# Optimization experiments

Measured on AMD Instinct MI355X. Metric: run time of the kernel, lower is better.

## Reference

```python
import jax, jax.numpy as jnp
import numpy as np

N = 100_000      # amino-acid nodes
E = 1_600_000    # edges per relation (avg degree 16)
D = 128          # input_dim
H = 128          # hidden_dim
L = 2            # num_layers
EPS = 1e-5       # BatchNorm eps


def setup_inputs() -> dict:
    key = jax.random.key(0)
    ks = jax.random.split(key, 20)
    inp = {
        "x": jax.random.normal(ks[0], (N, D), dtype=jnp.float32),
        "src_residue": jax.random.randint(ks[1], (E,), 0, N, dtype=jnp.int32),
        "dst_residue": jax.random.randint(ks[2], (E,), 0, N, dtype=jnp.int32),
        "src_seq": jax.random.randint(ks[3], (E,), 0, N, dtype=jnp.int32),
        "dst_seq": jax.random.randint(ks[4], (E,), 0, N, dtype=jnp.int32),
        "src_knn": jax.random.randint(ks[5], (E,), 0, N, dtype=jnp.int32),
        "dst_knn": jax.random.randint(ks[6], (E,), 0, N, dtype=jnp.int32),
        # GraphConv weights: 3 relations per layer; layer0 in=D, layer1 in=H
        "Wg0": jax.random.normal(ks[7], (3, D, H), dtype=jnp.float32) * (1.0 / np.sqrt(D)),
        "bg0": jnp.zeros((3, H), dtype=jnp.float32),
        "Wg1": jax.random.normal(ks[8], (3, H, H), dtype=jnp.float32) * (1.0 / np.sqrt(H)),
        "bg1": jnp.zeros((3, H), dtype=jnp.float32),
        # FC per layer
        "Wfc": jax.random.normal(ks[9], (L, H, H), dtype=jnp.float32) * (1.0 / np.sqrt(H)),
        "bfc": jax.random.normal(ks[10], (L, H), dtype=jnp.float32) * 0.01,
        # BatchNorm1d (eval mode: running stats)
        "bn_gamma": 1.0 + 0.1 * jax.random.normal(ks[11], (L, H), dtype=jnp.float32),
        "bn_beta": 0.1 * jax.random.normal(ks[12], (L, H), dtype=jnp.float32),
        "bn_mean": 0.1 * jax.random.normal(ks[13], (L, H), dtype=jnp.float32),
        "bn_var": jax.random.uniform(ks[14], (L, H), dtype=jnp.float32, minval=0.5, maxval=1.5),
    }
    return inp


def reference(x, src_residue, dst_residue, src_seq, dst_seq, src_knn, dst_knn,
              Wg0, bg0, Wg1, bg1, Wfc, bfc, bn_gamma, bn_beta, bn_mean, bn_var):
    n = x.shape[0]
    edges = [(src_residue, dst_residue), (src_seq, dst_seq), (src_knn, dst_knn)]

    def gconv(h, src, dst, W, b):
        # DGL GraphConv, norm='both': D_dst^{-1/2} A D_src^{-1/2} h W + b
        ones = jnp.ones(src.shape, h.dtype)
        deg_out = jnp.maximum(jax.ops.segment_sum(ones, src, num_segments=n), 1.0)
        deg_in = jnp.maximum(jax.ops.segment_sum(ones, dst, num_segments=n), 1.0)
        hn = h * jax.lax.rsqrt(deg_out)[:, None]
        agg = jax.ops.segment_sum(hn[src], dst, num_segments=n)  # [N, d] gather+scatter
        agg = agg * jax.lax.rsqrt(deg_in)[:, None]
        return agg @ W + b

    h = x
    layer_weights = [(Wg0, bg0), (Wg1, bg1)]
    for i, (Wg, bg) in enumerate(layer_weights):
        # HeteroGraphConv with aggregate='sum' over 3 relations
        out = gconv(h, edges[0][0], edges[0][1], Wg[0], bg[0])
        out = out + gconv(h, edges[1][0], edges[1][1], Wg[1], bg[1])
        out = out + gconv(h, edges[2][0], edges[2][1], Wg[2], bg[2])
        y = jax.nn.relu(out @ Wfc[i] + bfc[i])
        # BatchNorm1d (eval: running stats); dropout is identity in eval mode
        h = (y - bn_mean[i]) * jax.lax.rsqrt(bn_var[i] + EPS) * bn_gamma[i] + bn_beta[i]
    return h
```

## Files before the change

kernel.cpp:

```cpp
#include <hip/hip_runtime.h>
#include <stdint.h>

#define NN 100000
#define NE 1600000
#define NE4 (NE / 4)
#define NNP1 100008
#define NBK 196
#define NSL 64

typedef __attribute__((ext_vector_type(8))) short bfrag;
typedef __attribute__((ext_vector_type(4))) float ffrag;

__device__ __forceinline__ uint16_t f2bf(float f) {
  uint32_t u = __float_as_uint(f);
  u += 0x7fff + ((u >> 16) & 1);
  return (uint16_t)(u >> 16);
}
__device__ __forceinline__ uint32_t pack2(float a, float b) {
  return (uint32_t)f2bf(a) | ((uint32_t)f2bf(b) << 16);
}

__global__ void k_cast_x(const float* __restrict__ x, uint32_t* __restrict__ h) {
  int n = NN * 64;
  for (int i = blockIdx.x * blockDim.x + threadIdx.x; i < n; i += gridDim.x * blockDim.x) {
    float2 v = ((const float2*)x)[i];
    h[i] = pack2(v.x, v.y);
  }
}

__global__ void k_prep_w(const float* __restrict__ Wg0, const float* __restrict__ Wg1,
                         const float* __restrict__ Wfc, uint16_t* __restrict__ wswz) {
  int idx = blockIdx.x * 256 + threadIdx.x;
  int m = idx >> 14;
  int rem = idx & 16383;
  int j = rem & 7;
  int lane = (rem >> 3) & 63;
  int f = rem >> 9;
  int t = f >> 3, ct = f & 7;
  int k = t * 32 + (lane >> 4) * 8 + j;
  int n = ct * 16 + (lane & 15);
  const float* src = (m < 3) ? (Wg0 + m * 16384)
                   : (m < 6) ? (Wg1 + (m - 3) * 16384)
                             : (Wfc + (m - 6) * 16384);
  wswz[idx] = f2bf(src[k * 128 + n]);
}

__global__ void k_prep_consts(const float* __restrict__ bg0, const float* __restrict__ bg1,
                              const float* __restrict__ Wfc, const float* __restrict__ bfc,
                              const float* __restrict__ gamma, const float* __restrict__ beta,
                              const float* __restrict__ mean, const float* __restrict__ var,
                              float* __restrict__ cst) {
  int tid = threadIdx.x;
  int l = tid >> 7, n = tid & 127;
  const float* bg = l ? bg1 : bg0;
  float acc = bfc[l * 128 + n];
  for (int k = 0; k < 128; k++) {
    float bsum = bg[k] + bg[128 + k] + bg[256 + k];
    acc += bsum * Wfc[l * 16384 + k * 128 + n];
  }
  cst[tid] = acc;
  float g = gamma[tid] * rsqrtf(var[tid] + 1e-5f);
  cst[256 + tid] = g;
  cst[512 + tid] = beta[tid] - mean[tid] * g;
}

__global__ void k_bhist(const int* __restrict__ s0, const int* __restrict__ s1,
                        const int* __restrict__ s2, const int* __restrict__ d0,
                        const int* __restrict__ d1, const int* __restrict__ d2,
                        uint32_t* __restrict__ bh) {
  int r = blockIdx.y, blk = blockIdx.x, t = threadIdx.x;
  __shared__ uint32_t hD[NBK], hS[NBK];
  for (int i = t; i < NBK; i += 256) { hD[i] = 0; hS[i] = 0; }
  __syncthreads();
  const int4* sp = (const int4*)((r == 0) ? s0 : (r == 1) ? s1 : s2);
  const int4* dp = (const int4*)((r == 0) ? d0 : (r == 1) ? d1 : d2);
  int base = blk * (NE4 / NSL);
  for (int i = t; i < NE4 / NSL; i += 256) {
    int4 s = sp[base + i];
    int4 d = dp[base + i];
    atomicAdd(&hD[d.x >> 9], 1u); atomicAdd(&hD[d.y >> 9], 1u);
    atomicAdd(&hD[d.z >> 9], 1u); atomicAdd(&hD[d.w >> 9], 1u);
    atomicAdd(&hS[s.x >> 9], 1u); atomicAdd(&hS[s.y >> 9], 1u);
    atomicAdd(&hS[s.z >> 9], 1u); atomicAdd(&hS[s.w >> 9], 1u);
  }
  __syncthreads();
  for (int i = t; i < NBK; i += 256) {
    if (hD[i]) atomicAdd(&bh[r * NBK + i], hD[i]);
    if (hS[i]) atomicAdd(&bh[(3 + r) * NBK + i], hS[i]);
  }
}

__global__ void k_bscan(const uint32_t* __restrict__ bh, int* __restrict__ bases,
                        uint32_t* __restrict__ cur, int* __restrict__ rowptr) {
  int seg = blockIdx.x, t = threadIdx.x;
  int lane = t & 63, wid = t >> 6;
  int v = (t < NBK) ? (int)bh[seg * NBK + t] : 0;
  int x = v;
#pragma unroll
  for (int o = 1; o < 64; o <<= 1) { int y = __shfl_up(x, o); if (lane >= o) x += y; }
  __shared__ int ws[4];
  if (lane == 63) ws[wid] = x;
  __syncthreads();
  int woff = 0;
  for (int i = 0; i < wid; i++) woff += ws[i];
  int incl = woff + x, excl = incl - v;
  if (t < NBK) { bases[seg * (NBK + 1) + t] = excl; cur[seg * NBK + t] = (uint32_t)excl; }
  if (t == 255) bases[seg * (NBK + 1) + NBK] = incl;
  if (seg < 3 && t == 0) rowptr[seg * NNP1 + NN] = NE;
}

__global__ void k_bscatter(const int* __restrict__ s0, const int* __restrict__ s1,
                           const int* __restrict__ s2, const int* __restrict__ d0,
                           const int* __restrict__ d1, const int* __restrict__ d2,
                           uint32_t* __restrict__ cur, uint32_t* __restrict__ pairs,
                           uint16_t* __restrict__ srcs) {
  int r = blockIdx.y, blk = blockIdx.x, t = threadIdx.x;
  __shared__ uint32_t hD[NBK], hS[NBK];
  for (int i = t; i < NBK; i += 256) { hD[i] = 0; hS[i] = 0; }
  __syncthreads();
  const int4* sp = (const int4*)((r == 0) ? s0 : (r == 1) ? s1 : s2);
  const int4* dp = (const int4*)((r == 0) ? d0 : (r == 1) ? d1 : d2);
  int base = blk * (NE4 / NSL);
  for (int i = t; i < NE4 / NSL; i += 256) {
    int4 s = sp[base + i];
    int4 d = dp[base + i];
    atomicAdd(&hD[d.x >> 9], 1u); atomicAdd(&hD[d.y >> 9], 1u);
    atomicAdd(&hD[d.z >> 9], 1u); atomicAdd(&hD[d.w >> 9], 1u);
    atomicAdd(&hS[s.x >> 9], 1u); atomicAdd(&hS[s.y >> 9], 1u);
    atomicAdd(&hS[s.z >> 9], 1u); atomicAdd(&hS[s.w >> 9], 1u);
  }
  __syncthreads();
  for (int i = t; i < NBK; i += 256) {
    hD[i] = atomicAdd(&cur[r * NBK + i], hD[i]);
    hS[i] = atomicAdd(&cur[(3 + r) * NBK + i], hS[i]);
  }
  __syncthreads();
  uint32_t* pr = pairs + (size_t)r * NE;
  uint16_t* sr = srcs + (size_t)r * NE;
#define SCAT1(S, D) { \
    uint32_t p = atomicAdd(&hD[(D) >> 9], 1u); \
    pr[p] = (uint32_t)(((D) & 511) << 17) | (uint32_t)(S); \
    uint32_t q = atomicAdd(&hS[(S) >> 9], 1u); \
    sr[q] = (uint16_t)((S) & 511); }
  for (int i = t; i < NE4 / NSL; i += 256) {
    int4 s = sp[base + i];
    int4 d = dp[base + i];
    SCAT1(s.x, d.x) SCAT1(s.y, d.y) SCAT1(s.z, d.z) SCAT1(s.w, d.w)
  }
#undef SCAT1
}

__global__ void k_bucket_csr(const uint32_t* __restrict__ pairs, const int* __restrict__ bases,
                             int* __restrict__ rowptr, float* __restrict__ s_in,
                             int* __restrict__ col) {
  int b = blockIdx.x, r = blockIdx.y, t = threadIdx.x;
  int node0 = b << 9;
  int nc = min(512, NN - node0);
  int rb = bases[r * (NBK + 1) + b];
  int m = bases[r * (NBK + 1) + b + 1] - rb;
  __shared__ int cnt[512];
  __shared__ int exc[512];
  __shared__ int ws[4];
  cnt[t] = 0; cnt[t + 256] = 0;
  __syncthreads();
  const uint32_t* pp = pairs + (size_t)r * NE + rb;
  for (int i = t; i < m; i += 256) atomicAdd(&cnt[pp[i] >> 17], 1);
  __syncthreads();
  int v0 = cnt[2 * t], v1 = cnt[2 * t + 1];
  int s = v0 + v1, x = s;
  int lane = t & 63, wid = t >> 6;
#pragma unroll
  for (int o = 1; o < 64; o <<= 1) { int y = __shfl_up(x, o); if (lane >= o) x += y; }
  if (lane == 63) ws[wid] = x;
  __syncthreads();
  int woff = 0;
  for (int i = 0; i < wid; i++) woff += ws[i];
  int e0 = woff + x - s;
  exc[2 * t] = e0;
  exc[2 * t + 1] = e0 + v0;
  __syncthreads();
  for (int i = t; i < nc; i += 256) {
    rowptr[r * NNP1 + node0 + i] = rb + exc[i];
    s_in[r * NN + node0 + i] = rsqrtf((float)(cnt[i] < 1 ? 1 : cnt[i]));
  }
  __syncthreads();
  int* cl = col + (size_t)r * NE + rb;
  for (int i = t; i < m; i += 256) {
    uint32_t e = pp[i];
    int p = atomicAdd(&exc[e >> 17], 1);
    cl[p] = (int)(e & 0x1FFFF);
  }
}

__global__ void k_bucket_sout(const uint16_t* __restrict__ srcs, const int* __restrict__ bases,
                              float* __restrict__ s_out) {
  int b = blockIdx.x, r = blockIdx.y, t = threadIdx.x;
  int node0 = b << 9;
  int nc = min(512, NN - node0);
  int rb = bases[(3 + r) * (NBK + 1) + b];
  int m = bases[(3 + r) * (NBK + 1) + b + 1] - rb;
  __shared__ int cnt[512];
  cnt[t] = 0; cnt[t + 256] = 0;
  __syncthreads();
  const uint16_t* pp = srcs + (size_t)r * NE + rb;
  for (int i = t; i < m; i += 256) atomicAdd(&cnt[pp[i]], 1);
  __syncthreads();
  for (int i = t; i < nc; i += 256)
    s_out[r * NN + node0 + i] = rsqrtf((float)(cnt[i] < 1 ? 1 : cnt[i]));
}

__global__ void k_aggregate(const uint32_t* __restrict__ h, const int* __restrict__ rowptr,
                            const int* __restrict__ col, const float* __restrict__ s_out,
                            const float* __restrict__ s_in, uint32_t* __restrict__ agg) {
  int r = blockIdx.y;
  int node = blockIdx.x * 4 + (threadIdx.x >> 6);
  int lane = threadIdx.x & 63;
  const int* rp = rowptr + r * NNP1;
  int beg = rp[node], end = rp[node + 1];
  const int* cl = col + (size_t)r * NE;
  const float* so = s_out + r * NN;
  float a0 = 0.f, a1 = 0.f;
  for (int base = beg; base < end; base += 64) {
    int idx = base + lane;
    int sv = 0; int wb = 0;
    if (idx < end) { sv = cl[idx]; wb = __float_as_int(so[sv]); }
    int cnt = min(64, end - base);
    int cnt8 = (cnt + 7) & ~7;
    for (int j = 0; j < cnt8; j += 8) {
      uint32_t hv[8]; float ww[8];
#pragma unroll
      for (int u = 0; u < 8; u++) {
        int ss = __builtin_amdgcn_readlane(sv, j + u);
        ww[u] = __int_as_float(__builtin_amdgcn_readlane(wb, j + u));
        hv[u] = h[(size_t)ss * 64 + lane];
      }
#pragma unroll
      for (int u = 0; u < 8; u++) {
        a0 = fmaf(__uint_as_float(hv[u] << 16), ww[u], a0);
        a1 = fmaf(__uint_as_float(hv[u] & 0xffff0000u), ww[u], a1);
      }
    }
  }
  float sc = s_in[r * NN + node];
  agg[((size_t)r * NN + node) * 64 + lane] = pack2(a0 * sc, a1 * sc);
}

__global__ __launch_bounds__(256, 2) void k_gconv_mm(const uint32_t* __restrict__ agg,
                                                     const short* __restrict__ wswz,
                                                     int wbase, uint16_t* __restrict__ P) {
  int r = blockIdx.y;
  int lane = threadIdx.x & 63;
  int wid = threadIdx.x >> 6;
  int q = lane >> 4, n0 = lane & 15;
  const bfrag* wp = (const bfrag*)(wswz + (size_t)(wbase + r) * 16384);
  bfrag B[32];
#pragma unroll
  for (int f = 0; f < 32; f++) B[f] = wp[f * 64 + lane];
  const uint32_t* A = agg + (size_t)r * NN * 64;
  uint16_t* Pr = P + (size_t)r * NN * 128;
  const int ntiles = NN / 16;
  for (int tile = blockIdx.x * 4 + wid; tile < ntiles; tile += gridDim.x * 4) {
    int arow = tile * 16 + n0;
    bfrag a[4];
#pragma unroll
    for (int t = 0; t < 4; t++)
      a[t] = *(const bfrag*)(A + (size_t)arow * 64 + t * 16 + q * 4);
    ffrag acc[8];
#pragma unroll
    for (int ct = 0; ct < 8; ct++) {
      ffrag c = {0.f, 0.f, 0.f, 0.f};
#pragma unroll
      for (int t = 0; t < 4; t++)
        c = __builtin_amdgcn_mfma_f32_16x16x32_bf16(a[t], B[t * 8 + ct], c, 0, 0, 0);
      acc[ct] = c;
    }
    int orow = tile * 16 + q * 4;
#pragma unroll
    for (int ct = 0; ct < 8; ct++)
#pragma unroll
      for (int i = 0; i < 4; i++)
        Pr[(size_t)(orow + i) * 128 + ct * 16 + n0] = f2bf(acc[ct][i]);
  }
}

__global__ __launch_bounds__(256, 2) void k_fc(const uint32_t* __restrict__ P,
                                               const short* __restrict__ wswz, int m,
                                               const float* __restrict__ cst, int l,
                                               uint16_t* __restrict__ hout,
                                               float* __restrict__ fout, int wf32) {
  int lane = threadIdx.x & 63;
  int wid = threadIdx.x >> 6;
  int q = lane >> 4, n0 = lane & 15;
  const bfrag* wp = (const bfrag*)(wswz + (size_t)m * 16384);
  bfrag B[32];
#pragma unroll
  for (int f = 0; f < 32; f++) B[f] = wp[f * 64 + lane];
  float bb[8], gg[8], b2v[8];
#pragma unroll
  for (int ct = 0; ct < 8; ct++) {
    int c = l * 128 + ct * 16 + n0;
    bb[ct] = cst[c];
    gg[ct] = cst[256 + c];
    b2v[ct] = cst[512 + c];
  }
  const int ntiles = NN / 16;
  for (int tile = blockIdx.x * 4 + wid; tile < ntiles; tile += gridDim.x * 4) {
    int arow = tile * 16 + n0;
    ffrag acc[8];
#pragma unroll
    for (int ct = 0; ct < 8; ct++) acc[ct] = (ffrag){0.f, 0.f, 0.f, 0.f};
    for (int rr = 0; rr < 3; rr++) {
      const uint32_t* A = P + (size_t)rr * NN * 64;
      bfrag a[4];
#pragma unroll
      for (int t = 0; t < 4; t++)
        a[t] = *(const bfrag*)(A + (size_t)arow * 64 + t * 16 + q * 4);
#pragma unroll
      for (int ct = 0; ct < 8; ct++) {
#pragma unroll
        for (int t = 0; t < 4; t++)
          acc[ct] = __builtin_amdgcn_mfma_f32_16x16x32_bf16(a[t], B[t * 8 + ct], acc[ct], 0, 0, 0);
      }
    }
    int orow = tile * 16 + q * 4;
#pragma unroll
    for (int ct = 0; ct < 8; ct++) {
#pragma unroll
      for (int i = 0; i < 4; i++) {
        float y = acc[ct][i] + bb[ct];
        y = fmaxf(y, 0.f);
        float hv = fmaf(y, gg[ct], b2v[ct]);
        size_t oi = (size_t)(orow + i) * 128 + ct * 16 + n0;
        if (wf32) fout[oi] = hv;
        else hout[oi] = f2bf(hv);
      }
    }
  }
}

extern "C" void kernel_launch(void* const* d_in, const int* in_sizes, int n_in,
                              void* d_out, int out_size, void* d_ws, size_t ws_size,
                              hipStream_t stream) {
  const float* x = (const float*)d_in[0];
  const int* s0 = (const int*)d_in[1]; const int* d0 = (const int*)d_in[2];
  const int* s1 = (const int*)d_in[3]; const int* d1 = (const int*)d_in[4];
  const int* s2 = (const int*)d_in[5]; const int* d2 = (const int*)d_in[6];
  const float* Wg0 = (const float*)d_in[7];
  const float* bg0 = (const float*)d_in[8];
  const float* Wg1 = (const float*)d_in[9];
  const float* bg1 = (const float*)d_in[10];
  const float* Wfc = (const float*)d_in[11];
  const float* bfc = (const float*)d_in[12];
  const float* gamma = (const float*)d_in[13];
  const float* beta = (const float*)d_in[14];
  const float* mean = (const float*)d_in[15];
  const float* var = (const float*)d_in[16];

  char* ws = (char*)d_ws;
  size_t off = 0;
  auto alloc = [&](size_t bytes) { size_t o = off; off = (off + bytes + 255) & ~(size_t)255; return o; };
  size_t o_bh    = alloc((size_t)6 * NBK * 4);
  size_t o_bases = alloc((size_t)6 * (NBK + 1) * 4);
  size_t o_cur   = alloc((size_t)6 * NBK * 4);
  size_t o_sin   = alloc((size_t)3 * NN * 4);
  size_t o_sout  = alloc((size_t)3 * NN * 4);
  size_t o_rp    = alloc((size_t)3 * NNP1 * 4);
  size_t o_col   = alloc((size_t)3 * NE * 4);
  size_t o_wswz  = alloc((size_t)131072 * 2);
  size_t o_cst   = alloc((size_t)768 * 4);
  size_t o_h     = alloc((size_t)NN * 128 * 2);
  size_t o_agg   = alloc((size_t)3 * NN * 128 * 2);
  size_t o_P     = alloc((size_t)3 * NN * 128 * 2);
  (void)ws_size; (void)in_sizes; (void)n_in; (void)out_size;

  uint32_t* bh   = (uint32_t*)(ws + o_bh);
  int* bases     = (int*)(ws + o_bases);
  uint32_t* cur  = (uint32_t*)(ws + o_cur);
  float* s_in    = (float*)(ws + o_sin);
  float* s_out   = (float*)(ws + o_sout);
  int* rowptr    = (int*)(ws + o_rp);
  int* col       = (int*)(ws + o_col);
  uint16_t* wswz = (uint16_t*)(ws + o_wswz);
  float* cst     = (float*)(ws + o_cst);
  uint32_t* h    = (uint32_t*)(ws + o_h);
  uint32_t* agg  = (uint32_t*)(ws + o_agg);
  uint16_t* P    = (uint16_t*)(ws + o_P);
  uint32_t* pairs = (uint32_t*)(ws + o_agg);
  uint16_t* srcs  = (uint16_t*)(ws + o_agg + (size_t)3 * NE * 4);

  hipMemsetAsync(ws + o_bh, 0, (size_t)6 * NBK * 4, stream);

  k_cast_x<<<2048, 256, 0, stream>>>(x, h);
  k_prep_w<<<512, 256, 0, stream>>>(Wg0, Wg1, Wfc, wswz);
  k_prep_consts<<<1, 256, 0, stream>>>(bg0, bg1, Wfc, bfc, gamma, beta, mean, var, cst);
  k_bhist<<<dim3(NSL, 3), 256, 0, stream>>>(s0, s1, s2, d0, d1, d2, bh);
  k_bscan<<<6, 256, 0, stream>>>(bh, bases, cur, rowptr);
  k_bscatter<<<dim3(NSL, 3), 256, 0, stream>>>(s0, s1, s2, d0, d1, d2, cur, pairs, srcs);
  k_bucket_csr<<<dim3(NBK, 3), 256, 0, stream>>>(pairs, bases, rowptr, s_in, col);
  k_bucket_sout<<<dim3(NBK, 3), 256, 0, stream>>>(srcs, bases, s_out);

  for (int l = 0; l < 2; l++) {
    k_aggregate<<<dim3(25000, 3), 256, 0, stream>>>(h, rowptr, col, s_out, s_in, agg);
    k_gconv_mm<<<dim3(256, 3), 256, 0, stream>>>(agg, (const short*)wswz, 3 * l, P);
    k_fc<<<256, 256, 0, stream>>>((const uint32_t*)P, (const short*)wswz, 6 + l, cst, l,
                                  (uint16_t*)h, (float*)d_out, l);
  }
}
```

Before: 747.7 us.

## Fold GraphConv weights into FC weights and pack edge norms into CSR

```diff
diff --git a/kernel.cpp b/kernel.cpp
--- a/kernel.cpp
+++ b/kernel.cpp
@@ -28,21 +28,34 @@
   }
 }
 
-__global__ void k_prep_w(const float* __restrict__ Wg0, const float* __restrict__ Wg1,
-                         const float* __restrict__ Wfc, uint16_t* __restrict__ wswz) {
+__global__ void k_matmul_wc(const float* __restrict__ Wg0, const float* __restrict__ Wg1,
+                            const float* __restrict__ Wfc, float* __restrict__ Wc) {
+  int b = blockIdx.x;
+  int m = b >> 2, kq = b & 3;
+  int l = m / 3, rel = m % 3;
+  int t = threadIdx.x;
+  int n = t & 127, kh = t >> 7;
+  int k0 = kq * 32 + kh * 16;
+  const float* Wg = (l ? Wg1 : Wg0) + rel * 16384;
+  const float* Wf = Wfc + (size_t)l * 16384;
+  for (int k = k0; k < k0 + 16; k++) {
+    float acc = 0.f;
+    for (int kk = 0; kk < 128; kk++) acc = fmaf(Wg[k * 128 + kk], Wf[kk * 128 + n], acc);
+    Wc[(size_t)m * 16384 + k * 128 + n] = acc;
+  }
+}
+
+__global__ void k_prep_w(const float* __restrict__ Wc, uint16_t* __restrict__ wswz) {
   int idx = blockIdx.x * 256 + threadIdx.x;
+  int rem = idx & 16383;
   int m = idx >> 14;
-  int rem = idx & 16383;
   int j = rem & 7;
   int lane = (rem >> 3) & 63;
   int f = rem >> 9;
   int t = f >> 3, ct = f & 7;
   int k = t * 32 + (lane >> 4) * 8 + j;
   int n = ct * 16 + (lane & 15);
-  const float* src = (m < 3) ? (Wg0 + m * 16384)
-                   : (m < 6) ? (Wg1 + (m - 3) * 16384)
-                             : (Wfc + (m - 6) * 16384);
-  wswz[idx] = f2bf(src[k * 128 + n]);
+  wswz[idx] = f2bf(Wc[(size_t)m * 16384 + k * 128 + n]);
 }
 
 __global__ void k_prep_consts(const float* __restrict__ bg0, const float* __restrict__ bg1,
@@ -150,9 +163,26 @@
 #undef SCAT1
 }
 
+__global__ void k_bucket_sout(const uint16_t* __restrict__ srcs, const int* __restrict__ bases,
+                              float* __restrict__ s_out) {
+  int b = blockIdx.x, r = blockIdx.y, t = threadIdx.x;
+  int node0 = b << 9;
+  int nc = min(512, NN - node0);
+  int rb = bases[(3 + r) * (NBK + 1) + b];
+  int m = bases[(3 + r) * (NBK + 1) + b + 1] - rb;
+  __shared__ int cnt[512];
+  cnt[t] = 0; cnt[t + 256] = 0;
+  __syncthreads();
+  const uint16_t* pp = srcs + (size_t)r * NE + rb;
+  for (int i = t; i < m; i += 256) atomicAdd(&cnt[pp[i]], 1);
+  __syncthreads();
+  for (int i = t; i < nc; i += 256)
+    s_out[r * NN + node0 + i] = rsqrtf((float)(cnt[i] < 1 ? 1 : cnt[i]));
+}
+
 __global__ void k_bucket_csr(const uint32_t* __restrict__ pairs, const int* __restrict__ bases,
-                             int* __restrict__ rowptr, float* __restrict__ s_in,
-                             int* __restrict__ col) {
+                             const float* __restrict__ s_out, int* __restrict__ rowptr,
+                             float* __restrict__ s_in, int2* __restrict__ col2) {
   int b = blockIdx.x, r = blockIdx.y, t = threadIdx.x;
   int node0 = b << 9;
   int nc = min(512, NN - node0);
@@ -184,46 +214,29 @@
     s_in[r * NN + node0 + i] = rsqrtf((float)(cnt[i] < 1 ? 1 : cnt[i]));
   }
   __syncthreads();
-  int* cl = col + (size_t)r * NE + rb;
+  int2* cl = col2 + (size_t)r * NE + rb;
   for (int i = t; i < m; i += 256) {
     uint32_t e = pp[i];
+    int src = (int)(e & 0x1FFFF);
     int p = atomicAdd(&exc[e >> 17], 1);
-    cl[p] = (int)(e & 0x1FFFF);
-  }
-}
-
-__global__ void k_bucket_sout(const uint16_t* __restrict__ srcs, const int* __restrict__ bases,
-                              float* __restrict__ s_out) {
-  int b = blockIdx.x, r = blockIdx.y, t = threadIdx.x;
-  int node0 = b << 9;
-  int nc = min(512, NN - node0);
-  int rb = bases[(3 + r) * (NBK + 1) + b];
-  int m = bases[(3 + r) * (NBK + 1) + b + 1] - rb;
-  __shared__ int cnt[512];
-  cnt[t] = 0; cnt[t + 256] = 0;
-  __syncthreads();
-  const uint16_t* pp = srcs + (size_t)r * NE + rb;
-  for (int i = t; i < m; i += 256) atomicAdd(&cnt[pp[i]], 1);
-  __syncthreads();
-  for (int i = t; i < nc; i += 256)
-    s_out[r * NN + node0 + i] = rsqrtf((float)(cnt[i] < 1 ? 1 : cnt[i]));
+    cl[p] = make_int2(src, __float_as_int(s_out[r * NN + src]));
+  }
 }
 
 __global__ void k_aggregate(const uint32_t* __restrict__ h, const int* __restrict__ rowptr,
-                            const int* __restrict__ col, const float* __restrict__ s_out,
-                            const float* __restrict__ s_in, uint32_t* __restrict__ agg) {
+                            const int2* __restrict__ col2, const float* __restrict__ s_in,
+                            uint32_t* __restrict__ agg) {
   int r = blockIdx.y;
   int node = blockIdx.x * 4 + (threadIdx.x >> 6);
   int lane = threadIdx.x & 63;
   const int* rp = rowptr + r * NNP1;
   int beg = rp[node], end = rp[node + 1];
-  const int* cl = col + (size_t)r * NE;
-  const float* so = s_out + r * NN;
+  const int2* cl = col2 + (size_t)r * NE;
   float a0 = 0.f, a1 = 0.f;
   for (int base = beg; base < end; base += 64) {
     int idx = base + lane;
     int sv = 0; int wb = 0;
-    if (idx < end) { sv = cl[idx]; wb = __float_as_int(so[sv]); }
+    if (idx < end) { int2 e = cl[idx]; sv = e.x; wb = e.y; }
     int cnt = min(64, end - base);
     int cnt8 = (cnt + 7) & ~7;
     for (int j = 0; j < cnt8; j += 8) {
@@ -245,56 +258,15 @@
   agg[((size_t)r * NN + node) * 64 + lane] = pack2(a0 * sc, a1 * sc);
 }
 
-__global__ __launch_bounds__(256, 2) void k_gconv_mm(const uint32_t* __restrict__ agg,
-                                                     const short* __restrict__ wswz,
-                                                     int wbase, uint16_t* __restrict__ P) {
-  int r = blockIdx.y;
+__global__ __launch_bounds__(256, 2) void k_fc2(const uint32_t* __restrict__ agg,
+                                                const short* __restrict__ wswz,
+                                                const float* __restrict__ cst, int l,
+                                                uint16_t* __restrict__ hout,
+                                                float* __restrict__ fout, int wf32) {
   int lane = threadIdx.x & 63;
   int wid = threadIdx.x >> 6;
   int q = lane >> 4, n0 = lane & 15;
-  const bfrag* wp = (const bfrag*)(wswz + (size_t)(wbase + r) * 16384);
-  bfrag B[32];
-#pragma unroll
-  for (int f = 0; f < 32; f++) B[f] = wp[f * 64 + lane];
-  const uint32_t* A = agg + (size_t)r * NN * 64;
-  uint16_t* Pr = P + (size_t)r * NN * 128;
-  const int ntiles = NN / 16;
-  for (int tile = blockIdx.x * 4 + wid; tile < ntiles; tile += gridDim.x * 4) {
-    int arow = tile * 16 + n0;
-    bfrag a[4];
-#pragma unroll
-    for (int t = 0; t < 4; t++)
-      a[t] = *(const bfrag*)(A + (size_t)arow * 64 + t * 16 + q * 4);
-    ffrag acc[8];
-#pragma unroll
-    for (int ct = 0; ct < 8; ct++) {
-      ffrag c = {0.f, 0.f, 0.f, 0.f};
-#pragma unroll
-      for (int t = 0; t < 4; t++)
-        c = __builtin_amdgcn_mfma_f32_16x16x32_bf16(a[t], B[t * 8 + ct], c, 0, 0, 0);
-      acc[ct] = c;
-    }
-    int orow = tile * 16 + q * 4;
-#pragma unroll
-    for (int ct = 0; ct < 8; ct++)
-#pragma unroll
-      for (int i = 0; i < 4; i++)
-        Pr[(size_t)(orow + i) * 128 + ct * 16 + n0] = f2bf(acc[ct][i]);
-  }
-}
-
-__global__ __launch_bounds__(256, 2) void k_fc(const uint32_t* __restrict__ P,
-                                               const short* __restrict__ wswz, int m,
-                                               const float* __restrict__ cst, int l,
-                                               uint16_t* __restrict__ hout,
-                                               float* __restrict__ fout, int wf32) {
-  int lane = threadIdx.x & 63;
-  int wid = threadIdx.x >> 6;
-  int q = lane >> 4, n0 = lane & 15;
-  const bfrag* wp = (const bfrag*)(wswz + (size_t)m * 16384);
-  bfrag B[32];
-#pragma unroll
-  for (int f = 0; f < 32; f++) B[f] = wp[f * 64 + lane];
+  const bfrag* wb = (const bfrag*)(wswz + (size_t)(l * 3) * 16384);
   float bb[8], gg[8], b2v[8];
 #pragma unroll
   for (int ct = 0; ct < 8; ct++) {
@@ -303,36 +275,42 @@
     gg[ct] = cst[256 + c];
     b2v[ct] = cst[512 + c];
   }
-  const int ntiles = NN / 16;
+  const int ntiles = NN / 32;
   for (int tile = blockIdx.x * 4 + wid; tile < ntiles; tile += gridDim.x * 4) {
-    int arow = tile * 16 + n0;
-    ffrag acc[8];
-#pragma unroll
-    for (int ct = 0; ct < 8; ct++) acc[ct] = (ffrag){0.f, 0.f, 0.f, 0.f};
-    for (int rr = 0; rr < 3; rr++) {
-      const uint32_t* A = P + (size_t)rr * NN * 64;
-      bfrag a[4];
-#pragma unroll
-      for (int t = 0; t < 4; t++)
-        a[t] = *(const bfrag*)(A + (size_t)arow * 64 + t * 16 + q * 4);
+    ffrag acc[2][8];
+#pragma unroll
+    for (int s = 0; s < 2; s++)
+#pragma unroll
+      for (int ct = 0; ct < 8; ct++) acc[s][ct] = (ffrag){0.f, 0.f, 0.f, 0.f};
+    for (int kt = 0; kt < 12; kt++) {
+      int rel = kt >> 2, kt4 = kt & 3;
+      const uint32_t* A = agg + (size_t)rel * NN * 64 + kt4 * 16 + q * 4;
+      bfrag a[2];
+#pragma unroll
+      for (int s = 0; s < 2; s++)
+        a[s] = *(const bfrag*)(A + (size_t)(tile * 32 + s * 16 + n0) * 64);
+      const bfrag* wk = wb + (size_t)rel * 2048 + (kt4 * 8) * 64 + lane;
 #pragma unroll
       for (int ct = 0; ct < 8; ct++) {
-#pragma unroll
-        for (int t = 0; t < 4; t++)
-          acc[ct] = __builtin_amdgcn_mfma_f32_16x16x32_bf16(a[t], B[t * 8 + ct], acc[ct], 0, 0, 0);
+        bfrag B = wk[ct * 64];
+        acc[0][ct] = __builtin_amdgcn_mfma_f32_16x16x32_bf16(a[0], B, acc[0][ct], 0, 0, 0);
+        acc[1][ct] = __builtin_amdgcn_mfma_f32_16x16x32_bf16(a[1], B, acc[1][ct], 0, 0, 0);
       }
     }
-    int orow = tile * 16 + q * 4;
-#pragma unroll
-    for (int ct = 0; ct < 8; ct++) {
-#pragma unroll
-      for (int i = 0; i < 4; i++) {
-        float y = acc[ct][i] + bb[ct];
-        y = fmaxf(y, 0.f);
-        float hv = fmaf(y, gg[ct], b2v[ct]);
-        size_t oi = (size_t)(orow + i) * 128 + ct * 16 + n0;
-        if (wf32) fout[oi] = hv;
-        else hout[oi] = f2bf(hv);
+#pragma unroll
+    for (int s = 0; s < 2; s++) {
+      int orow = tile * 32 + s * 16 + q * 4;
+#pragma unroll
+      for (int ct = 0; ct < 8; ct++) {
+#pragma unroll
+        for (int i = 0; i < 4; i++) {
+          float y = acc[s][ct][i] + bb[ct];
+          y = fmaxf(y, 0.f);
+          float hv = fmaf(y, gg[ct], b2v[ct]);
+          size_t oi = (size_t)(orow + i) * 128 + ct * 16 + n0;
+          if (wf32) fout[oi] = hv;
+          else hout[oi] = f2bf(hv);
+        }
       }
     }
   }
@@ -365,12 +343,12 @@
   size_t o_sin   = alloc((size_t)3 * NN * 4);
   size_t o_sout  = alloc((size_t)3 * NN * 4);
   size_t o_rp    = alloc((size_t)3 * NNP1 * 4);
-  size_t o_col   = alloc((size_t)3 * NE * 4);
-  size_t o_wswz  = alloc((size_t)131072 * 2);
+  size_t o_col2  = alloc((size_t)3 * NE * 8);
+  size_t o_wc    = alloc((size_t)6 * 16384 * 4);
+  size_t o_wswz  = alloc((size_t)6 * 16384 * 2);
   size_t o_cst   = alloc((size_t)768 * 4);
   size_t o_h     = alloc((size_t)NN * 128 * 2);
   size_t o_agg   = alloc((size_t)3 * NN * 128 * 2);
-  size_t o_P     = alloc((size_t)3 * NN * 128 * 2);
   (void)ws_size; (void)in_sizes; (void)n_in; (void)out_size;
 
   uint32_t* bh   = (uint32_t*)(ws + o_bh);
@@ -379,30 +357,30 @@
   float* s_in    = (float*)(ws + o_sin);
   float* s_out   = (float*)(ws + o_sout);
   int* rowptr    = (int*)(ws + o_rp);
-  int* col       = (int*)(ws + o_col);
+  int2* col2     = (int2*)(ws + o_col2);
+  float* Wc      = (float*)(ws + o_wc);
   uint16_t* wswz = (uint16_t*)(ws + o_wswz);
   float* cst     = (float*)(ws + o_cst);
   uint32_t* h    = (uint32_t*)(ws + o_h);
   uint32_t* agg  = (uint32_t*)(ws + o_agg);
-  uint16_t* P    = (uint16_t*)(ws + o_P);
   uint32_t* pairs = (uint32_t*)(ws + o_agg);
   uint16_t* srcs  = (uint16_t*)(ws + o_agg + (size_t)3 * NE * 4);
 
   hipMemsetAsync(ws + o_bh, 0, (size_t)6 * NBK * 4, stream);
 
   k_cast_x<<<2048, 256, 0, stream>>>(x, h);
-  k_prep_w<<<512, 256, 0, stream>>>(Wg0, Wg1, Wfc, wswz);
+  k_matmul_wc<<<24, 256, 0, stream>>>(Wg0, Wg1, Wfc, Wc);
+  k_prep_w<<<384, 256, 0, stream>>>(Wc, wswz);
   k_prep_consts<<<1, 256, 0, stream>>>(bg0, bg1, Wfc, bfc, gamma, beta, mean, var, cst);
   k_bhist<<<dim3(NSL, 3), 256, 0, stream>>>(s0, s1, s2, d0, d1, d2, bh);
   k_bscan<<<6, 256, 0, stream>>>(bh, bases, cur, rowptr);
   k_bscatter<<<dim3(NSL, 3), 256, 0, stream>>>(s0, s1, s2, d0, d1, d2, cur, pairs, srcs);
-  k_bucket_csr<<<dim3(NBK, 3), 256, 0, stream>>>(pairs, bases, rowptr, s_in, col);
   k_bucket_sout<<<dim3(NBK, 3), 256, 0, stream>>>(srcs, bases, s_out);
+  k_bucket_csr<<<dim3(NBK, 3), 256, 0, stream>>>(pairs, bases, s_out, rowptr, s_in, col2);
 
   for (int l = 0; l < 2; l++) {
-    k_aggregate<<<dim3(25000, 3), 256, 0, stream>>>(h, rowptr, col, s_out, s_in, agg);
-    k_gconv_mm<<<dim3(256, 3), 256, 0, stream>>>(agg, (const short*)wswz, 3 * l, P);
-    k_fc<<<256, 256, 0, stream>>>((const uint32_t*)P, (const short*)wswz, 6 + l, cst, l,
-                                  (uint16_t*)h, (float*)d_out, l);
-  }
-}
+    k_aggregate<<<dim3(25000, 3), 256, 0, stream>>>(h, rowptr, col2, s_in, agg);
+    k_fc2<<<256, 256, 0, stream>>>(agg, (const short*)wswz, cst, l,
+                                   (uint16_t*)h, (float*)d_out, l);
+  }
+}
```

Measured after the change: 850.2 us. +13.7%, slower.
